# Optimization experiments

Measured on AMD Instinct MI355X. Metric: run time of the kernel, lower is better.

## Reference

```python
import jax, jax.numpy as jnp
import numpy as np

EMBED_DIM = 1024
NUM_HEADS = 16
HEAD_DIM = EMBED_DIM // NUM_HEADS  # 64
NUM_QUBITS = 6  # ceil(log2(64))


def _bit_indices(dim, nq):
    idx = np.arange(dim)
    pairs = []
    for i in range(nq):
        mask = 1 << i
        pairs.append((np.where((idx & mask) == 0)[0], np.where((idx & mask) != 0)[0]))
    return pairs

_BIT_PAIRS = _bit_indices(HEAD_DIM, NUM_QUBITS)


def quantum_layer(x, theta, phi, preW, preb, postW, postb):
    # x: [..., HEAD_DIM]
    shape = x.shape
    xf = x.reshape(-1, HEAD_DIM)
    res = xf @ preW.T + preb
    for i, (i0, i1) in enumerate(_BIT_PAIRS):
        c = jnp.cos(theta[i])
        s = jnp.sin(theta[i])
        cp = jnp.cos(phi[i])  # real part of exp(1j*phi)
        x0 = res[:, i0]
        x1 = res[:, i1]
        res = res.at[:, i0].set(c * x0 - s * x1)
        res = res.at[:, i1].set((s * x0 + c * x1) * cp)
    out = res @ postW.T + postb + xf
    return out.reshape(shape)


def setup_inputs() -> dict:
    key = jax.random.key(0)
    ks = jax.random.split(key, 24)
    B, S, E = 4, 2048, EMBED_DIM
    d = {}
    d['query'] = jax.random.normal(ks[0], (B, S, E), dtype=jnp.float32)
    d['key'] = jax.random.normal(ks[1], (B, S, E), dtype=jnp.float32)
    d['value'] = jax.random.normal(ks[2], (B, S, E), dtype=jnp.float32)
    scale = 1.0 / np.sqrt(E)
    d['wq'] = jax.random.normal(ks[3], (E, E), dtype=jnp.float32) * scale
    d['bq'] = jnp.zeros((E,), jnp.float32)
    d['wk'] = jax.random.normal(ks[4], (E, E), dtype=jnp.float32) * scale
    d['bk'] = jnp.zeros((E,), jnp.float32)
    d['wv'] = jax.random.normal(ks[5], (E, E), dtype=jnp.float32) * scale
    d['bv'] = jnp.zeros((E,), jnp.float32)
    d['wo'] = jax.random.normal(ks[6], (E, E), dtype=jnp.float32) * scale
    d['bo'] = jnp.zeros((E,), jnp.float32)
    hd = HEAD_DIM
    hscale = 1.0 / np.sqrt(hd)
    d['q_theta'] = jax.random.normal(ks[7], (NUM_QUBITS,), dtype=jnp.float32) * 0.02
    d['q_phi'] = jax.random.normal(ks[8], (NUM_QUBITS,), dtype=jnp.float32) * 0.02
    d['q_preW'] = jax.random.normal(ks[9], (hd, hd), dtype=jnp.float32) * hscale
    d['q_preb'] = jnp.zeros((hd,), jnp.float32)
    d['q_postW'] = jax.random.normal(ks[10], (hd, hd), dtype=jnp.float32) * hscale
    d['q_postb'] = jnp.zeros((hd,), jnp.float32)
    d['k_theta'] = jax.random.normal(ks[11], (NUM_QUBITS,), dtype=jnp.float32) * 0.02
    d['k_phi'] = jax.random.normal(ks[12], (NUM_QUBITS,), dtype=jnp.float32) * 0.02
    d['k_preW'] = jax.random.normal(ks[13], (hd, hd), dtype=jnp.float32) * hscale
    d['k_preb'] = jnp.zeros((hd,), jnp.float32)
    d['k_postW'] = jax.random.normal(ks[14], (hd, hd), dtype=jnp.float32) * hscale
    d['k_postb'] = jnp.zeros((hd,), jnp.float32)
    return d


def reference(query, key, value, wq, bq, wk, bk, wv, bv, wo, bo,
              q_theta, q_phi, q_preW, q_preb, q_postW, q_postb,
              k_theta, k_phi, k_preW, k_preb, k_postW, k_postb):
    B, Sq, E = query.shape
    H, Dh = NUM_HEADS, HEAD_DIM
    q = (query @ wq.T + bq).reshape(B, Sq, H, Dh).transpose(0, 2, 1, 3)
    k = (key @ wk.T + bk).reshape(B, -1, H, Dh).transpose(0, 2, 1, 3)
    v = (value @ wv.T + bv).reshape(B, -1, H, Dh).transpose(0, 2, 1, 3)
    q = quantum_layer(q, q_theta, q_phi, q_preW, q_preb, q_postW, q_postb)
    k = quantum_layer(k, k_theta, k_phi, k_preW, k_preb, k_postW, k_postb)
    scores = jnp.einsum('bhqd,bhkd->bhqk', q, k) / jnp.sqrt(jnp.float32(Dh))
    attn = jax.nn.softmax(scores, axis=-1)
    out = jnp.einsum('bhqk,bhkd->bhqd', attn, v)
    out = out.transpose(0, 2, 1, 3).reshape(B, Sq, E)
    return out @ wo.T + bo
```

## Files before the change

### kernel.cpp

```cpp
#include <hip/hip_runtime.h>
#include <cstdint>

typedef unsigned short u16;
typedef __attribute__((ext_vector_type(4))) float f32x4;
typedef __attribute__((ext_vector_type(8))) short s16x8;
typedef __attribute__((ext_vector_type(2))) unsigned int u32x2;
typedef __attribute__((ext_vector_type(4))) unsigned int u32x4;
typedef __attribute__((ext_vector_type(4))) unsigned short u16x4;

#define MFMA16(a,b,c) __builtin_amdgcn_mfma_f32_16x16x32_bf16((a),(b),(c),0,0,0)

__device__ __forceinline__ u16 f2bf(float x) {
  unsigned u = __builtin_bit_cast(unsigned, x);
  unsigned r = (u + 0x7fffu + ((u >> 16) & 1u)) >> 16;
  return (u16)r;
}
__device__ __forceinline__ unsigned cvt_pk_bf16(float lo, float hi) {
  unsigned r;
  asm volatile("v_cvt_pk_bf16_f32 %0, %1, %2" : "=v"(r) : "v"(lo), "v"(hi));
  return r;
}
__device__ __forceinline__ int swz(int row, int colb) {
  return (row * 128 + colb) ^ ((row & 7) << 4);
}
__device__ __forceinline__ void glds16(const u16* g, u16* l) {
  __builtin_amdgcn_global_load_lds(
      (const __attribute__((address_space(1))) void*)g,
      (__attribute__((address_space(3))) void*)l, 16, 0, 0);
}

__global__ void cvt_f32_bf16_2(const float* __restrict__ inA, u16* __restrict__ outA,
                               const float* __restrict__ inB, u16* __restrict__ outB, int n) {
  const float* in = blockIdx.y ? inB : inA;
  u16* out = blockIdx.y ? outB : outA;
  const int i = (blockIdx.x * 256 + threadIdx.x) * 4;
  if (i + 3 < n) {
    const float4 v = *(const float4*)(in + i);
    u32x2 o2;
    o2[0] = cvt_pk_bf16(v.x, v.y);
    o2[1] = cvt_pk_bf16(v.z, v.w);
    *(u32x2*)(out + i) = o2;
  }
}

__global__ __launch_bounds__(256) void build_quantum2(
    const float* __restrict__ thq, const float* __restrict__ phq,
    const float* __restrict__ preWq, const float* __restrict__ prebq,
    const float* __restrict__ postWq, const float* __restrict__ postbq,
    float* __restrict__ Aoutq, float* __restrict__ coutq,
    const float* __restrict__ thk, const float* __restrict__ phk,
    const float* __restrict__ preWk, const float* __restrict__ prebk,
    const float* __restrict__ postWk, const float* __restrict__ postbk,
    float* __restrict__ Aoutk, float* __restrict__ coutk) {
  const int zq = blockIdx.x == 0;
  const float* theta = zq ? thq : thk;
  const float* phi   = zq ? phq : phk;
  const float* preW  = zq ? preWq : preWk;
  const float* preb  = zq ? prebq : prebk;
  const float* postW = zq ? postWq : postWk;
  const float* postb = zq ? postbq : postbk;
  float* Aout  = zq ? Aoutq : Aoutk;
  float* cout_ = zq ? coutq : coutk;

  __shared__ float R[64][65];
  __shared__ float W[64][65];
  __shared__ float T[64][65];
  __shared__ float rbv[64];
  const int t = threadIdx.x;

  float m00[6], m01[6], m10[6], m11[6];
  #pragma unroll
  for (int i = 0; i < 6; ++i) {
    const float cth = cosf(theta[i]), sth = sinf(theta[i]), cph = cosf(phi[i]);
    m00[i] = cth; m01[i] = -sth; m10[i] = sth * cph; m11[i] = cth * cph;
  }
  for (int ii = t; ii < 4096; ii += 256) {
    const int r = ii >> 6, cc = ii & 63;
    float p = 1.f;
    #pragma unroll
    for (int i = 0; i < 6; ++i) {
      const int rb_ = (r >> i) & 1, cb = (cc >> i) & 1;
      p *= rb_ ? (cb ? m11[i] : m10[i]) : (cb ? m01[i] : m00[i]);
    }
    R[r][cc] = p;
    W[r][cc] = preW[ii];
  }
  __syncthreads();
  for (int ii = t; ii < 4096; ii += 256) {
    const int d = ii >> 6, j = ii & 63;
    float acc = 0.f;
    #pragma unroll
    for (int e = 0; e < 64; ++e) acc += R[d][e] * W[e][j];
    T[d][j] = acc;
  }
  if (t < 64) {
    float acc = 0.f;
    #pragma unroll
    for (int e = 0; e < 64; ++e) acc += R[t][e] * preb[e];
    rbv[t] = acc;
  }
  __syncthreads();
  for (int ii = t; ii < 4096; ii += 256) W[ii >> 6][ii & 63] = postW[ii];
  __syncthreads();
  for (int ii = t; ii < 4096; ii += 256) {
    const int d = ii >> 6, j = ii & 63;
    float acc = (d == j) ? 1.f : 0.f;
    #pragma unroll
    for (int e = 0; e < 64; ++e) acc += W[d][e] * T[e][j];
    Aout[ii] = acc;
  }
  if (t < 64) {
    float acc = postb[t];
    #pragma unroll
    for (int e = 0; e < 64; ++e) acc += W[t][e] * rbv[e];
    cout_[t] = acc;
  }
}

__global__ __launch_bounds__(256) void fold_weight2(
    const float* __restrict__ Aq, const float* __restrict__ cq,
    const float* __restrict__ wq, const float* __restrict__ bq,
    u16* __restrict__ Wqp, float* __restrict__ bqp,
    const float* __restrict__ Ak, const float* __restrict__ ck,
    const float* __restrict__ wk, const float* __restrict__ bk,
    u16* __restrict__ Wkp, float* __restrict__ bkp) {
  const int zq = blockIdx.z == 0;
  const float* Ap   = zq ? Aq : Ak;
  const float* cvec = zq ? cq : ck;
  const float* W    = zq ? wq : wk;
  const float* bin  = zq ? bq : bk;
  u16* Wout   = zq ? Wqp : Wkp;
  float* bout = zq ? bqp : bkp;
  const float scale = zq ? 0.18033688f : 1.0f;

  __shared__ float sW[64][64];
  __shared__ float sA[64][64];
  const int h = blockIdx.y, k0 = blockIdx.x * 64;
  const int t = threadIdx.x;
  for (int ii = t; ii < 4096; ii += 256) {
    const int e = ii >> 6, kk = ii & 63;
    sW[e][kk] = W[(size_t)(h * 64 + e) * 1024 + k0 + kk];
    sA[e][kk] = Ap[ii];
  }
  __syncthreads();
  for (int ii = t; ii < 4096; ii += 256) {
    const int d = ii >> 6, kk = ii & 63;
    float acc = 0.f;
    #pragma unroll
    for (int e = 0; e < 64; ++e) acc += sA[d][e] * sW[e][kk];
    Wout[(size_t)(h * 64 + d) * 1024 + k0 + kk] = f2bf(acc * scale);
  }
  if (blockIdx.x == 0 && t < 64) {
    const int d = t;
    float acc = cvec[d];
    for (int e = 0; e < 64; ++e) acc += sA[d][e] * bin[h * 64 + e];
    bout[h * 64 + d] = acc * scale;
  }
}

__global__ __launch_bounds__(256, 2) void qkv_proj(
    const float* __restrict__ qsrc, const float* __restrict__ ksrc, const float* __restrict__ vsrc,
    const u16* __restrict__ Wq, const u16* __restrict__ Wk, const u16* __restrict__ Wv,
    const float* __restrict__ bq, const float* __restrict__ bk, const float* __restrict__ bv,
    u16* __restrict__ Qt, u16* __restrict__ Kt, u16* __restrict__ VtT) {
  const int z = blockIdx.z;
  const float* Af = (z == 0) ? qsrc : (z == 1) ? ksrc : vsrc;
  const u16* Bw   = (z == 0) ? Wq : (z == 1) ? Wk : Wv;
  const float* bias = (z == 0) ? bq : (z == 1) ? bk : bv;
  u16* outB = (z == 0) ? Qt : (z == 1) ? Kt : VtT;
  const int K = 1024;

  __shared__ u16 AsBuf[9216];
  __shared__ u16 Bs[2][8192];
  const int t = threadIdx.x;
  const int l = t & 63, w = t >> 6;
  const int g = l >> 4, c = l & 15;
  const int wr = w >> 1, wc = w & 1;
  const int m0 = blockIdx.x * 128, n0 = blockIdx.y * 128;

  const int lrow8 = l >> 3;
  const int gcolsw = ((l & 7) ^ lrow8) * 8;
  const int lbase = w * 512;

  auto glds_tile = [&](const u16* src, u16* ldsbuf, int rbase, int kk) {
    #pragma unroll
    for (int i = 0; i < 4; ++i) {
      const int grow = i * 32 + w * 8 + lrow8;
      glds16(src + (size_t)(rbase + grow) * K + kk + gcolsw, ldsbuf + i * 2048 + lbase);
    }
  };

  const int rowA32 = t >> 3, colA32 = (t & 7) * 8;
  float4 fa[4][2];
  auto issue_A = [&](int kk) {
    #pragma unroll
    for (int i2 = 0; i2 < 4; ++i2) {
      const float* p = Af + (size_t)(m0 + rowA32 + i2 * 32) * K + kk + colA32;
      fa[i2][0] = *(const float4*)p;
      fa[i2][1] = *(const float4*)(p + 4);
    }
  };

  f32x4 acc[4][4];
  #pragma unroll
  for (int i = 0; i < 4; ++i)
    #pragma unroll
    for (int j = 0; j < 4; ++j) acc[i][j] = f32x4{0.f, 0.f, 0.f, 0.f};

  issue_A(0);
  glds_tile(Bw, Bs[0], n0, 0);

  int cur = 0;
  for (int kk = 0; kk < K; kk += 64) {
    #pragma unroll
    for (int i2 = 0; i2 < 4; ++i2) {
      u32x4 o4;
      o4[0] = cvt_pk_bf16(fa[i2][0].x, fa[i2][0].y);
      o4[1] = cvt_pk_bf16(fa[i2][0].z, fa[i2][0].w);
      o4[2] = cvt_pk_bf16(fa[i2][1].x, fa[i2][1].y);
      o4[3] = cvt_pk_bf16(fa[i2][1].z, fa[i2][1].w);
      *(u32x4*)&AsBuf[(rowA32 + i2 * 32) * 72 + colA32] = o4;
    }
    __syncthreads();
    const int nk = kk + 64;
    if (nk < K) {
      glds_tile(Bw, Bs[cur ^ 1], n0, nk);
      issue_A(nk);
    }

    s16x8 af[4][2], bfr[4][2];
    #pragma unroll
    for (int mi = 0; mi < 4; ++mi)
      #pragma unroll
      for (int kt = 0; kt < 2; ++kt)
        af[mi][kt] = *(const s16x8*)&AsBuf[(wr * 64 + mi * 16 + c) * 72 + kt * 32 + g * 8];
    {
      const char* Bb = (const char*)Bs[cur];
      #pragma unroll
      for (int ni = 0; ni < 4; ++ni) {
        const int rr = wc * 64 + ni * 16 + c;
        #pragma unroll
        for (int kt = 0; kt < 2; ++kt)
          bfr[ni][kt] = *(const s16x8*)(Bb + rr * 128 + (((kt * 4 + g) ^ (c & 7)) << 4));
      }
    }
    #pragma unroll
    for (int kt = 0; kt < 2; ++kt)
      #pragma unroll
      for (int mi = 0; mi < 4; ++mi)
        #pragma unroll
        for (int ni = 0; ni < 4; ++ni)
          acc[mi][ni] = MFMA16(af[mi][kt], bfr[ni][kt], acc[mi][ni]);
    __syncthreads();
    cur ^= 1;
  }

  #pragma unroll
  for (int ni = 0; ni < 4; ++ni) {
    const int n = n0 + wc * 64 + ni * 16 + c;
    const float bb = bias[n];
    #pragma unroll
    for (int mi = 0; mi < 4; ++mi) {
      const int mb = m0 + wr * 64 + mi * 16 + g * 4;
      if (z == 2) {
        const int b = mb >> 11, sb = mb & 2047, h = n >> 6, d = n & 63;
        u16x4 pk;
        #pragma unroll
        for (int r = 0; r < 4; ++r) pk[r] = f2bf(acc[mi][ni][r] + bb);
        *(u16x4*)(outB + ((size_t)(b * 16 + h) * 64 + d) * 2048 + sb) = pk;
      } else {
        #pragma unroll
        for (int r = 0; r < 4; ++r) {
          const int m = mb + r;
          const int b = m >> 11, s = m & 2047, h = n >> 6, d = n & 63;
          outB[((size_t)((b * 16 + h) * 2048 + s)) * 64 + d] = f2bf(acc[mi][ni][r] + bb);
        }
      }
    }
  }
}

__global__ __launch_bounds__(256, 2) void gemm_out(
    const u16* __restrict__ Ab, const u16* __restrict__ Bw,
    const float* __restrict__ bias, float* __restrict__ outF, int M, int N, int K) {
  __shared__ u16 As[2][8192];
  __shared__ u16 Bs[2][8192];
  const int t = threadIdx.x;
  const int l = t & 63, w = t >> 6;
  const int g = l >> 4, c = l & 15;
  const int wr = w >> 1, wc = w & 1;
  const int m0 = blockIdx.x * 128, n0 = blockIdx.y * 128;

  const int lrow8 = l >> 3;
  const int gcolsw = ((l & 7) ^ lrow8) * 8;
  const int lbase = w * 512;

  auto glds_tile = [&](const u16* src, u16* ldsbuf, int rbase, int kk) {
    #pragma unroll
    for (int i = 0; i < 4; ++i) {
      const int grow = i * 32 + w * 8 + lrow8;
      glds16(src + (size_t)(rbase + grow) * K + kk + gcolsw, ldsbuf + i * 2048 + lbase);
    }
  };

  f32x4 acc[4][4];
  #pragma unroll
  for (int i = 0; i < 4; ++i)
    #pragma unroll
    for (int j = 0; j < 4; ++j) acc[i][j] = f32x4{0.f, 0.f, 0.f, 0.f};

  glds_tile(Ab, As[0], m0, 0);
  glds_tile(Bw, Bs[0], n0, 0);

  int cur = 0;
  for (int kk = 0; kk < K; kk += 64) {
    __syncthreads();
    const int nk = kk + 64;
    if (nk < K) {
      glds_tile(Ab, As[cur ^ 1], m0, nk);
      glds_tile(Bw, Bs[cur ^ 1], n0, nk);
    }
    s16x8 af[4][2], bfr[4][2];
    {
      const char* Ab2 = (const char*)As[cur];
      #pragma unroll
      for (int mi = 0; mi < 4; ++mi) {
        const int ar = wr * 64 + mi * 16 + c;
        #pragma unroll
        for (int kt = 0; kt < 2; ++kt)
          af[mi][kt] = *(const s16x8*)(Ab2 + ar * 128 + (((kt * 4 + g) ^ (c & 7)) << 4));
      }
      const char* Bb = (const char*)Bs[cur];
      #pragma unroll
      for (int ni = 0; ni < 4; ++ni) {
        const int rr = wc * 64 + ni * 16 + c;
        #pragma unroll
        for (int kt = 0; kt < 2; ++kt)
          bfr[ni][kt] = *(const s16x8*)(Bb + rr * 128 + (((kt * 4 + g) ^ (c & 7)) << 4));
      }
    }
    #pragma unroll
    for (int kt = 0; kt < 2; ++kt)
      #pragma unroll
      for (int mi = 0; mi < 4; ++mi)
        #pragma unroll
        for (int ni = 0; ni < 4; ++ni)
          acc[mi][ni] = MFMA16(af[mi][kt], bfr[ni][kt], acc[mi][ni]);
    __syncthreads();
    cur ^= 1;
  }

  #pragma unroll
  for (int ni = 0; ni < 4; ++ni) {
    const int n = n0 + wc * 64 + ni * 16 + c;
    const float bb = bias[n];
    #pragma unroll
    for (int mi = 0; mi < 4; ++mi) {
      const int mb = m0 + wr * 64 + mi * 16 + g * 4;
      #pragma unroll
      for (int r = 0; r < 4; ++r)
        outF[(size_t)(mb + r) * N + n] = acc[mi][ni][r] + bb;
    }
  }
}

__global__ __launch_bounds__(256, 2) void attn_fwd(
    const u16* __restrict__ Qg, const u16* __restrict__ Kg,
    const u16* __restrict__ Vtg, u16* __restrict__ Og) {
  __shared__ u16 Ks[64 * 64];
  __shared__ u16 Vs[64 * 64];
  __shared__ u16 Ps[4][32 * 64];
  const int t = threadIdx.x;
  const int l = t & 63, w = t >> 6;
  const int g = l >> 4, c = l & 15;
  const int bid = blockIdx.x;
  const int xcd = bid & 7, kk_ = bid >> 3;
  const int bh = ((kk_ >> 4) << 3) + xcd;
  const int qx = kk_ & 15;
  const size_t base = (size_t)bh * (2048 * 64);
  const int q0 = qx * 128 + w * 32;

  s16x8 qf[2][2];
  #pragma unroll
  for (int nt = 0; nt < 2; ++nt)
    #pragma unroll
    for (int kt = 0; kt < 2; ++kt)
      qf[nt][kt] = *(const s16x8*)(Qg + base + (size_t)(q0 + nt * 16 + c) * 64 + kt * 32 + g * 8);

  s16x8 onesf;
  #pragma unroll
  for (int j = 0; j < 8; ++j) onesf[j] = (short)0x3F80;

  f32x4 o[4][2];
  f32x4 ol[2];
  #pragma unroll
  for (int i = 0; i < 4; ++i) { o[i][0] = f32x4{0.f,0.f,0.f,0.f}; o[i][1] = f32x4{0.f,0.f,0.f,0.f}; }
  ol[0] = f32x4{0.f,0.f,0.f,0.f};
  ol[1] = f32x4{0.f,0.f,0.f,0.f};

  const int row1 = t >> 3, ch1 = t & 7;
  char* Pw = (char*)&Ps[w][0];
  char* Kb = (char*)Ks;
  char* Vb = (char*)Vs;

  s16x8 kreg[2], vreg[2];
  #pragma unroll
  for (int j = 0; j < 2; ++j) {
    const int row = row1 + 32 * j;
    kreg[j] = *(const s16x8*)(Kg + base + (size_t)row * 64 + ch1 * 8);
    vreg[j] = *(const s16x8*)(Vtg + base + (size_t)row * 2048 + ch1 * 8);
  }

  for (int it = 0; it < 32; ++it) {
    const int kv0 = it * 64;
    #pragma unroll
    for (int j = 0; j < 2; ++j) {
      const int row = row1 + 32 * j;
      *(s16x8*)(Kb + swz(row, ch1 * 16)) = kreg[j];
      *(s16x8*)(Vb + swz(row, ch1 * 16)) = vreg[j];
    }
    __syncthreads();
    if (it != 31) {
      const int kv0n = kv0 + 64;
      #pragma unroll
      for (int j = 0; j < 2; ++j) {
        const int row = row1 + 32 * j;
        kreg[j] = *(const s16x8*)(Kg + base + (size_t)(kv0n + row) * 64 + ch1 * 8);
        vreg[j] = *(const s16x8*)(Vtg + base + (size_t)row * 2048 + kv0n + ch1 * 8);
      }
    }

    f32x4 st[4][2];
    __builtin_amdgcn_s_setprio(1);
    #pragma unroll
    for (int mt = 0; mt < 4; ++mt) {
      const int kr = mt * 16 + c;
      const s16x8 k0 = *(const s16x8*)(Kb + swz(kr, g * 16));
      const s16x8 k1 = *(const s16x8*)(Kb + swz(kr, 64 + g * 16));
      #pragma unroll
      for (int nt = 0; nt < 2; ++nt) {
        f32x4 z = {0.f, 0.f, 0.f, 0.f};
        z = MFMA16(k0, qf[nt][0], z);
        z = MFMA16(k1, qf[nt][1], z);
        st[mt][nt] = z;
      }
    }
    __builtin_amdgcn_s_setprio(0);

    #pragma unroll
    for (int nt = 0; nt < 2; ++nt) {
      const int q32 = nt * 16 + c;
      #pragma unroll
      for (int mt = 0; mt < 4; ++mt) {
        const float p0 = exp2f(st[mt][nt][0]);
        const float p1 = exp2f(st[mt][nt][1]);
        const float p2 = exp2f(st[mt][nt][2]);
        const float p3 = exp2f(st[mt][nt][3]);
        u32x2 pv;
        pv[0] = cvt_pk_bf16(p0, p1);
        pv[1] = cvt_pk_bf16(p2, p3);
        *(u32x2*)(Pw + swz(q32, mt * 32 + g * 8)) = pv;
      }
    }
    asm volatile("s_waitcnt lgkmcnt(0)" ::: "memory");

    __builtin_amdgcn_s_setprio(1);
    #pragma unroll
    for (int kkb = 0; kkb < 2; ++kkb) {
      const s16x8 pb0 = *(const s16x8*)(Pw + swz(c,      kkb * 64 + g * 16));
      const s16x8 pb1 = *(const s16x8*)(Pw + swz(16 + c, kkb * 64 + g * 16));
      ol[0] = MFMA16(onesf, pb0, ol[0]);
      ol[1] = MFMA16(onesf, pb1, ol[1]);
      #pragma unroll
      for (int dt = 0; dt < 4; ++dt) {
        const s16x8 vfr = *(const s16x8*)(Vb + swz(dt * 16 + c, kkb * 64 + g * 16));
        o[dt][0] = MFMA16(vfr, pb0, o[dt][0]);
        o[dt][1] = MFMA16(vfr, pb1, o[dt][1]);
      }
    }
    __builtin_amdgcn_s_setprio(0);
    __syncthreads();
  }

  const int b = bh >> 4, h = bh & 15;
  #pragma unroll
  for (int nt = 0; nt < 2; ++nt) {
    const float inv = 1.0f / ol[nt][0];
    const int token = q0 + nt * 16 + c;
    u16* orow = Og + ((size_t)(b * 2048 + token)) * 1024 + h * 64;
    #pragma unroll
    for (int dt = 0; dt < 4; ++dt) {
      u32x2 pv;
      pv[0] = cvt_pk_bf16(o[dt][nt][0] * inv, o[dt][nt][1] * inv);
      pv[1] = cvt_pk_bf16(o[dt][nt][2] * inv, o[dt][nt][3] * inv);
      *(u32x2*)(orow + dt * 16 + g * 4) = pv;
    }
  }
}

extern "C" void kernel_launch(void* const* d_in, const int* in_sizes, int n_in,
                              void* d_out, int out_size, void* d_ws, size_t ws_size,
                              hipStream_t stream) {
  (void)in_sizes; (void)n_in; (void)out_size; (void)ws_size;
  const float* query   = (const float*)d_in[0];
  const float* key     = (const float*)d_in[1];
  const float* value   = (const float*)d_in[2];
  const float* wq      = (const float*)d_in[3];
  const float* bq      = (const float*)d_in[4];
  const float* wk      = (const float*)d_in[5];
  const float* bk      = (const float*)d_in[6];
  const float* wv      = (const float*)d_in[7];
  const float* bv      = (const float*)d_in[8];
  const float* wo      = (const float*)d_in[9];
  const float* bo      = (const float*)d_in[10];
  const float* q_theta = (const float*)d_in[11];
  const float* q_phi   = (const float*)d_in[12];
  const float* q_preW  = (const float*)d_in[13];
  const float* q_preb  = (const float*)d_in[14];
  const float* q_postW = (const float*)d_in[15];
  const float* q_postb = (const float*)d_in[16];
  const float* k_theta = (const float*)d_in[17];
  const float* k_phi   = (const float*)d_in[18];
  const float* k_preW  = (const float*)d_in[19];
  const float* k_preb  = (const float*)d_in[20];
  const float* k_postW = (const float*)d_in[21];
  const float* k_postb = (const float*)d_in[22];

  char* ws = (char*)d_ws;
  const size_t ACT = (size_t)8192 * 1024 * 2;
  u16* Qt  = (u16*)(ws + 0 * ACT);
  u16* Kt  = (u16*)(ws + 1 * ACT);
  u16* VtT = (u16*)(ws + 2 * ACT);
  u16* AO  = (u16*)(ws + 3 * ACT);
  char* wb = ws + 4 * ACT;
  const size_t WSZ = (size_t)1024 * 1024 * 2;
  u16* Wqp = (u16*)(wb);
  u16* Wkp = (u16*)(wb + WSZ);
  u16* Wvb = (u16*)(wb + 2 * WSZ);
  u16* Wob = (u16*)(wb + 3 * WSZ);
  float* bqp = (float*)(wb + 4 * WSZ);
  float* bkp = (float*)(wb + 4 * WSZ + 4096);
  float* Aq  = (float*)(wb + 4 * WSZ + 8192);
  float* Ak  = (float*)(wb + 4 * WSZ + 8192 + 16384);
  float* cq  = (float*)(wb + 4 * WSZ + 8192 + 32768);
  float* ck  = (float*)(wb + 4 * WSZ + 8192 + 32768 + 256);

  cvt_f32_bf16_2<<<dim3(1024, 2), 256, 0, stream>>>(wv, Wvb, wo, Wob, 1048576);
  build_quantum2<<<2, 256, 0, stream>>>(
      q_theta, q_phi, q_preW, q_preb, q_postW, q_postb, Aq, cq,
      k_theta, k_phi, k_preW, k_preb, k_postW, k_postb, Ak, ck);
  fold_weight2<<<dim3(16, 16, 2), 256, 0, stream>>>(
      Aq, cq, wq, bq, Wqp, bqp, Ak, ck, wk, bk, Wkp, bkp);

  qkv_proj<<<dim3(64, 8, 3), 256, 0, stream>>>(
      query, key, value, Wqp, Wkp, Wvb, bqp, bkp, bv, Qt, Kt, VtT);

  attn_fwd<<<1024, 256, 0, stream>>>(Qt, Kt, VtT, AO);

  gemm_out<<<dim3(64, 8), 256, 0, stream>>>(AO, Wob, bo, (float*)d_out, 8192, 1024, 1024);
}
```

Baseline: 246.6 us.

## Double query rows per warp in attention to reuse K/V tiles

Each warp now handles 64 query rows instead of 32, so a block covers 256 queries and the grid halves to 512 blocks. K fragments are loaded once per tile and reused across four query sub-tiles, and V fragments feed four MFMAs each, which cuts LDS reads and global K/V traffic per query. The trade-off is more accumulator registers, a larger P buffer in shared memory, and fewer blocks (512 across the GPU), which may lower occupancy and load balance.

```diff
diff --git a/kernel.cpp b/kernel.cpp
--- a/kernel.cpp
+++ b/kernel.cpp
@@ -369,20 +369,20 @@
     const u16* __restrict__ Vtg, u16* __restrict__ Og) {
   __shared__ u16 Ks[64 * 64];
   __shared__ u16 Vs[64 * 64];
-  __shared__ u16 Ps[4][32 * 64];
+  __shared__ u16 Ps[4][64 * 64];
   const int t = threadIdx.x;
   const int l = t & 63, w = t >> 6;
   const int g = l >> 4, c = l & 15;
   const int bid = blockIdx.x;
   const int xcd = bid & 7, kk_ = bid >> 3;
-  const int bh = ((kk_ >> 4) << 3) + xcd;
-  const int qx = kk_ & 15;
+  const int bh = ((kk_ >> 3) << 3) + xcd;
+  const int qx = kk_ & 7;
   const size_t base = (size_t)bh * (2048 * 64);
-  const int q0 = qx * 128 + w * 32;
-
-  s16x8 qf[2][2];
-  #pragma unroll
-  for (int nt = 0; nt < 2; ++nt)
+  const int q0 = qx * 256 + w * 64;
+
+  s16x8 qf[4][2];
+  #pragma unroll
+  for (int nt = 0; nt < 4; ++nt)
     #pragma unroll
     for (int kt = 0; kt < 2; ++kt)
       qf[nt][kt] = *(const s16x8*)(Qg + base + (size_t)(q0 + nt * 16 + c) * 64 + kt * 32 + g * 8);
@@ -391,12 +391,14 @@
   #pragma unroll
   for (int j = 0; j < 8; ++j) onesf[j] = (short)0x3F80;
 
-  f32x4 o[4][2];
-  f32x4 ol[2];
-  #pragma unroll
-  for (int i = 0; i < 4; ++i) { o[i][0] = f32x4{0.f,0.f,0.f,0.f}; o[i][1] = f32x4{0.f,0.f,0.f,0.f}; }
-  ol[0] = f32x4{0.f,0.f,0.f,0.f};
-  ol[1] = f32x4{0.f,0.f,0.f,0.f};
+  f32x4 o[4][4];
+  f32x4 ol[4];
+  #pragma unroll
+  for (int i = 0; i < 4; ++i) {
+    #pragma unroll
+    for (int j = 0; j < 4; ++j) o[i][j] = f32x4{0.f,0.f,0.f,0.f};
+    ol[i] = f32x4{0.f,0.f,0.f,0.f};
+  }
 
   const int row1 = t >> 3, ch1 = t & 7;
   char* Pw = (char*)&Ps[w][0];
@@ -430,35 +432,32 @@
       }
     }
 
-    f32x4 st[4][2];
-    __builtin_amdgcn_s_setprio(1);
+    s16x8 kf[4][2];
     #pragma unroll
     for (int mt = 0; mt < 4; ++mt) {
       const int kr = mt * 16 + c;
-      const s16x8 k0 = *(const s16x8*)(Kb + swz(kr, g * 16));
-      const s16x8 k1 = *(const s16x8*)(Kb + swz(kr, 64 + g * 16));
-      #pragma unroll
-      for (int nt = 0; nt < 2; ++nt) {
+      kf[mt][0] = *(const s16x8*)(Kb + swz(kr, g * 16));
+      kf[mt][1] = *(const s16x8*)(Kb + swz(kr, 64 + g * 16));
+    }
+
+    #pragma unroll
+    for (int nt = 0; nt < 4; ++nt) {
+      f32x4 st[4];
+      __builtin_amdgcn_s_setprio(1);
+      #pragma unroll
+      for (int mt = 0; mt < 4; ++mt) {
         f32x4 z = {0.f, 0.f, 0.f, 0.f};
-        z = MFMA16(k0, qf[nt][0], z);
-        z = MFMA16(k1, qf[nt][1], z);
-        st[mt][nt] = z;
-      }
-    }
-    __builtin_amdgcn_s_setprio(0);
-
-    #pragma unroll
-    for (int nt = 0; nt < 2; ++nt) {
+        z = MFMA16(kf[mt][0], qf[nt][0], z);
+        z = MFMA16(kf[mt][1], qf[nt][1], z);
+        st[mt] = z;
+      }
+      __builtin_amdgcn_s_setprio(0);
       const int q32 = nt * 16 + c;
       #pragma unroll
       for (int mt = 0; mt < 4; ++mt) {
-        const float p0 = exp2f(st[mt][nt][0]);
-        const float p1 = exp2f(st[mt][nt][1]);
-        const float p2 = exp2f(st[mt][nt][2]);
-        const float p3 = exp2f(st[mt][nt][3]);
         u32x2 pv;
-        pv[0] = cvt_pk_bf16(p0, p1);
-        pv[1] = cvt_pk_bf16(p2, p3);
+        pv[0] = cvt_pk_bf16(exp2f(st[mt][0]), exp2f(st[mt][1]));
+        pv[1] = cvt_pk_bf16(exp2f(st[mt][2]), exp2f(st[mt][3]));
         *(u32x2*)(Pw + swz(q32, mt * 32 + g * 8)) = pv;
       }
     }
@@ -467,15 +466,19 @@
     __builtin_amdgcn_s_setprio(1);
     #pragma unroll
     for (int kkb = 0; kkb < 2; ++kkb) {
-      const s16x8 pb0 = *(const s16x8*)(Pw + swz(c,      kkb * 64 + g * 16));
-      const s16x8 pb1 = *(const s16x8*)(Pw + swz(16 + c, kkb * 64 + g * 16));
-      ol[0] = MFMA16(onesf, pb0, ol[0]);
-      ol[1] = MFMA16(onesf, pb1, ol[1]);
+      s16x8 pb[4];
+      #pragma unroll
+      for (int nt = 0; nt < 4; ++nt)
+        pb[nt] = *(const s16x8*)(Pw + swz(nt * 16 + c, kkb * 64 + g * 16));
+      #pragma unroll
+      for (int nt = 0; nt < 4; ++nt)
+        ol[nt] = MFMA16(onesf, pb[nt], ol[nt]);
       #pragma unroll
       for (int dt = 0; dt < 4; ++dt) {
         const s16x8 vfr = *(const s16x8*)(Vb + swz(dt * 16 + c, kkb * 64 + g * 16));
-        o[dt][0] = MFMA16(vfr, pb0, o[dt][0]);
-        o[dt][1] = MFMA16(vfr, pb1, o[dt][1]);
+        #pragma unroll
+        for (int nt = 0; nt < 4; ++nt)
+          o[dt][nt] = MFMA16(vfr, pb[nt], o[dt][nt]);
       }
     }
     __builtin_amdgcn_s_setprio(0);
@@ -484,7 +487,7 @@
 
   const int b = bh >> 4, h = bh & 15;
   #pragma unroll
-  for (int nt = 0; nt < 2; ++nt) {
+  for (int nt = 0; nt < 4; ++nt) {
     const float inv = 1.0f / ol[nt][0];
     const int token = q0 + nt * 16 + c;
     u16* orow = Og + ((size_t)(b * 2048 + token)) * 1024 + h * 64;
@@ -555,7 +558,7 @@
   qkv_proj<<<dim3(64, 8, 3), 256, 0, stream>>>(
       query, key, value, Wqp, Wkp, Wvb, bqp, bkp, bv, Qt, Kt, VtT);
 
-  attn_fwd<<<1024, 256, 0, stream>>>(Qt, Kt, VtT, AO);
+  attn_fwd<<<512, 256, 0, stream>>>(Qt, Kt, VtT, AO);
 
   gemm_out<<<dim3(64, 8), 256, 0, stream>>>(AO, Wob, bo, (float*)d_out, 8192, 1024, 1024);
 }
```

Result: no change. 249.1 us (+1.0%).
